# Performance work log

Hardware: AMD Instinct MI355X
Metric: run time of the kernel (lower is better)

## Reference

```python
import jax, jax.numpy as jnp
import numpy as np


def setup_inputs() -> dict:
    key = jax.random.key(0)
    k1, k2, k3, k4 = jax.random.split(key, 4)
    N, F, E, M = 50000, 128, 1600000, 1024
    return {
        "molec_feature_vectures": jax.random.normal(k1, (N, F), dtype=jnp.float32),
        "W": jax.random.normal(k2, (F, F), dtype=jnp.float32),
        "mo_neighbour_indices": jax.random.randint(k3, (2, E), 0, N, dtype=jnp.int64),
        "mo_mol_id": jax.random.randint(k4, (E,), 0, M, dtype=jnp.int64),
        "n_output": M,
    }


def reference(molec_feature_vectures, W, mo_neighbour_indices, mo_mol_id, n_output):
    # Gather endpoint features for each neighbor pair: [E, F]
    fi = molec_feature_vectures[mo_neighbour_indices[0]]
    fj = molec_feature_vectures[mo_neighbour_indices[1]]
    # Symmetric bilinear form (mode='pes'): s_n = fi_n . (W + W^T) . fj_n
    Ws = W + W.T  # [F, F]
    # Fuse as (fi @ Ws) * fj summed over F to avoid a 3-operand einsum blowup
    scalars = jnp.einsum('ni,ij,nj->n', fi, Ws, fj)  # [E]
    # Segment-sum per molecule
    res = jax.ops.segment_sum(scalars, mo_mol_id, num_segments=n_output)  # [M]
    return res
```

## Files before the change

kernel.cpp:

```cpp
#include <hip/hip_runtime.h>
#include <hip/hip_bf16.h>

#define FDIM 128
#define BROWS 32
#define NBLK 128
#define NSLICE 32

typedef __attribute__((ext_vector_type(8))) short short8v;
typedef __attribute__((ext_vector_type(4))) float f32x4;
typedef __attribute__((ext_vector_type(2))) _Float16 half2v;

static __device__ __forceinline__ unsigned short f2bf(float x) {
    unsigned u = __float_as_uint(x);
    unsigned r = 0x7fffu + ((u >> 16) & 1u);
    return (unsigned short)((u + r) >> 16);
}
static __device__ __forceinline__ float bf2f(unsigned short h) {
    return __uint_as_float((unsigned)h << 16);
}
static __device__ __forceinline__ void split2(float v, short& h, short& l) {
    unsigned short hh = f2bf(v);
    h = (short)hh;
    l = (short)f2bf(v - bf2f(hh));
}

static __device__ __forceinline__ half2v u2h(unsigned u) {
    union { unsigned u; half2v h; } c; c.u = u; return c.h;
}
static __device__ __forceinline__ unsigned pack2h(float a, float b) {
    union { unsigned u; half2v h; } c;
    c.h[0] = (_Float16)a; c.h[1] = (_Float16)b; return c.u;
}
static __device__ __forceinline__ unsigned short f2h(float x) {
    union { unsigned short s; _Float16 h; } c; c.h = (_Float16)x; return c.s;
}
static __device__ __forceinline__ float fdot2(half2v a, half2v b, float c) {
#if defined(__has_builtin) && __has_builtin(__builtin_amdgcn_fdot2)
    return __builtin_amdgcn_fdot2(a, b, c, false);
#else
    return fmaf((float)a[1], (float)b[1], fmaf((float)a[0], (float)b[0], c));
#endif
}

__global__ void make_ws2(const float* __restrict__ W,
                         unsigned short* __restrict__ WsH,
                         unsigned short* __restrict__ WsL) {
    int idx = blockIdx.x * 256 + threadIdx.x;
    int i = idx >> 7, j = idx & 127;
    float w = W[idx] + W[j * 128 + i];
    short h, l;
    split2(w, h, l);
    WsH[idx] = (unsigned short)h;
    WsL[idx] = (unsigned short)l;
}

__global__ __launch_bounds__(512, 4) void gemm_mfma(
    const float* __restrict__ Fm,
    const unsigned short* __restrict__ WsH, const unsigned short* __restrict__ WsL,
    unsigned short* __restrict__ Gh, int N) {
    __shared__ __align__(16) unsigned short sH[128 * 136];
    __shared__ __align__(16) unsigned short sL[128 * 136];

    for (int k = threadIdx.x; k < 128 * 16; k += 512) {
        int i = k >> 4, g = k & 15;
        *(uint4*)((char*)sH + i * 272 + g * 16) =
            *(const uint4*)((const char*)WsH + i * 256 + g * 16);
        *(uint4*)((char*)sL + i * 272 + g * 16) =
            *(const uint4*)((const char*)WsL + i * 256 + g * 16);
    }
    __syncthreads();

    const int wid  = threadIdx.x >> 6;
    const int lane = threadIdx.x & 63;
    const int ar   = lane & 15;
    const int kg   = lane >> 4;
    const int row0 = blockIdx.x * 128 + wid * 16;
    const int gr   = row0 + ar;
    const bool rv  = gr < N;
    const float* fp = Fm + (size_t)gr * FDIM;

    f32x4 acc[8];
#pragma unroll
    for (int t = 0; t < 8; ++t) acc[t] = (f32x4){0.f, 0.f, 0.f, 0.f};

#pragma unroll
    for (int ks = 0; ks < 4; ++ks) {
        const int k0 = ks * 32 + kg * 8;
        float4 fa = make_float4(0.f, 0.f, 0.f, 0.f);
        float4 fb = make_float4(0.f, 0.f, 0.f, 0.f);
        if (rv) {
            fa = *(const float4*)(fp + k0);
            fb = *(const float4*)(fp + k0 + 4);
        }
        short8v ah, al;
        {
            short h, l;
            split2(fa.x, h, l); ah[0] = h; al[0] = l;
            split2(fa.y, h, l); ah[1] = h; al[1] = l;
            split2(fa.z, h, l); ah[2] = h; al[2] = l;
            split2(fa.w, h, l); ah[3] = h; al[3] = l;
            split2(fb.x, h, l); ah[4] = h; al[4] = l;
            split2(fb.y, h, l); ah[5] = h; al[5] = l;
            split2(fb.z, h, l); ah[6] = h; al[6] = l;
            split2(fb.w, h, l); ah[7] = h; al[7] = l;
        }
#pragma unroll
        for (int ct = 0; ct < 8; ++ct) {
            const short8v bh = *(const short8v*)(sH + (ct * 16 + ar) * 136 + k0);
            const short8v bl = *(const short8v*)(sL + (ct * 16 + ar) * 136 + k0);
            acc[ct] = __builtin_amdgcn_mfma_f32_16x16x32_bf16(ah, bh, acc[ct], 0, 0, 0);
            acc[ct] = __builtin_amdgcn_mfma_f32_16x16x32_bf16(ah, bl, acc[ct], 0, 0, 0);
            acc[ct] = __builtin_amdgcn_mfma_f32_16x16x32_bf16(al, bh, acc[ct], 0, 0, 0);
        }
    }

#pragma unroll
    for (int r = 0; r < 4; ++r) {
        const int orow = row0 + kg * 4 + r;
        if (orow < N) {
#pragma unroll
            for (int ct = 0; ct < 8; ++ct)
                Gh[(size_t)orow * FDIM + ct * 16 + ar] = f2h(acc[ct][r]);
        }
    }
}

__global__ __launch_bounds__(1024) void k_hist(const int* __restrict__ idx, int E,
                                               int nb, unsigned* __restrict__ M) {
    extern __shared__ unsigned cnt[];
    for (int i = threadIdx.x; i < nb; i += 1024) cnt[i] = 0;
    __syncthreads();
    int chunk = (E + NBLK - 1) / NBLK;
    int s = blockIdx.x * chunk;
    int e_end = min(E, s + chunk);
    for (int e = s + threadIdx.x; e < e_end; e += 1024) {
        int i1 = idx[E + e];
        atomicAdd(&cnt[i1 >> 5], 1u);
    }
    __syncthreads();
    for (int i = threadIdx.x; i < nb; i += 1024)
        M[(size_t)blockIdx.x * nb + i] = cnt[i];
}

__global__ __launch_bounds__(256) void k_mscan2(unsigned* __restrict__ M, int nb,
                                                unsigned* __restrict__ tot) {
    int b = blockIdx.x * 4 + (threadIdx.x >> 6);
    int lane = threadIdx.x & 63;
    if (b >= nb) return;
    unsigned m0 = M[(size_t)(2 * lane + 0) * nb + b];
    unsigned m1 = M[(size_t)(2 * lane + 1) * nb + b];
    unsigned s = m0 + m1;
    unsigned incl = s;
#pragma unroll
    for (int d = 1; d < 64; d <<= 1) {
        unsigned u = __shfl_up(incl, d, 64);
        if (lane >= d) incl += u;
    }
    unsigned run = incl - s;
    M[(size_t)(2 * lane + 0) * nb + b] = run; run += m0;
    M[(size_t)(2 * lane + 1) * nb + b] = run;
    if (lane == 63) tot[b] = incl;
}

__global__ __launch_bounds__(256) void k_bscan(const unsigned* __restrict__ tot, int nb,
                                               unsigned* __restrict__ bucketStart) {
    __shared__ unsigned wS[4];
    int t = threadIdx.x;
    unsigned v0, v1, v2, v3, v4, v5, v6, v7;
    int b0 = t * 8;
    v0 = (b0 + 0 < nb) ? tot[b0 + 0] : 0u;
    v1 = (b0 + 1 < nb) ? tot[b0 + 1] : 0u;
    v2 = (b0 + 2 < nb) ? tot[b0 + 2] : 0u;
    v3 = (b0 + 3 < nb) ? tot[b0 + 3] : 0u;
    v4 = (b0 + 4 < nb) ? tot[b0 + 4] : 0u;
    v5 = (b0 + 5 < nb) ? tot[b0 + 5] : 0u;
    v6 = (b0 + 6 < nb) ? tot[b0 + 6] : 0u;
    v7 = (b0 + 7 < nb) ? tot[b0 + 7] : 0u;
    unsigned l0 = 0, l1 = v0, l2 = l1 + v1, l3 = l2 + v2, l4 = l3 + v3,
             l5 = l4 + v4, l6 = l5 + v5, l7 = l6 + v6;
    unsigned s = l7 + v7;
    int lane = t & 63, wid = t >> 6;
    unsigned incl = s;
    for (int d = 1; d < 64; d <<= 1) {
        unsigned u = __shfl_up(incl, d, 64);
        if (lane >= d) incl += u;
    }
    if (lane == 63) wS[wid] = incl;
    __syncthreads();
    unsigned wOff = 0;
    for (int i = 0; i < wid; ++i) wOff += wS[i];
    unsigned base = wOff + incl - s;
    if (b0 + 0 < nb) bucketStart[b0 + 0] = base + l0;
    if (b0 + 1 < nb) bucketStart[b0 + 1] = base + l1;
    if (b0 + 2 < nb) bucketStart[b0 + 2] = base + l2;
    if (b0 + 3 < nb) bucketStart[b0 + 3] = base + l3;
    if (b0 + 4 < nb) bucketStart[b0 + 4] = base + l4;
    if (b0 + 5 < nb) bucketStart[b0 + 5] = base + l5;
    if (b0 + 6 < nb) bucketStart[b0 + 6] = base + l6;
    if (b0 + 7 < nb) bucketStart[b0 + 7] = base + l7;
    if (t == 255) bucketStart[nb] = base + s;
}

__global__ __launch_bounds__(1024) void k_scatter(const int* __restrict__ idx,
                                                  const int* __restrict__ mol, int E,
                                                  int nb, const unsigned* __restrict__ M,
                                                  const unsigned* __restrict__ bucketStart,
                                                  unsigned* __restrict__ sortedE) {
    extern __shared__ unsigned cur[];
    for (int i = threadIdx.x; i < nb; i += 1024)
        cur[i] = M[(size_t)blockIdx.x * nb + i] + bucketStart[i];
    __syncthreads();
    int chunk = (E + NBLK - 1) / NBLK;
    int s = blockIdx.x * chunk;
    int e_end = min(E, s + chunk);
    for (int e = s + threadIdx.x; e < e_end; e += 1024) {
        int i0 = idx[e];
        int i1 = idx[E + e];
        int m  = mol[e];
        int b  = i1 >> 5;
        int loc = i1 & 31;
        unsigned pos = atomicAdd(&cur[b], 1u);
        sortedE[pos] = (unsigned)i0 | ((unsigned)m << 16) | ((unsigned)loc << 26);
    }
}

__global__ __launch_bounds__(512, 6) void edge_kernel(
    const unsigned short* __restrict__ Gh, const float* __restrict__ Fm,
    const unsigned* __restrict__ sortedE, const unsigned* __restrict__ bucketStart,
    float* __restrict__ part, int N, int Mout) {
    __shared__ __align__(16) unsigned short sFrow[BROWS * FDIM];
    __shared__ float smol[1024];

    const int b = blockIdx.x;
    const int row0 = b * BROWS;
    const int nrow = min(BROWS, N - row0);

    for (int k = threadIdx.x; k < nrow * 16; k += 512) {
        int r = k >> 4, g = k & 15;
        const float4* src = (const float4*)(Fm + (size_t)(row0 + r) * FDIM + g * 8);
        float4 v0 = src[0], v1 = src[1];
        uint4 u;
        u.x = pack2h(v0.x, v0.y);
        u.y = pack2h(v0.z, v0.w);
        u.z = pack2h(v1.x, v1.y);
        u.w = pack2h(v1.z, v1.w);
        *(uint4*)(sFrow + r * FDIM + g * 8) = u;
    }
    for (int i = threadIdx.x; i < 1024; i += 512) smol[i] = 0.f;
    __syncthreads();

    const int s = (int)bucketStart[b];
    const int e_end = (int)bucketStart[b + 1];
    const int lane = threadIdx.x & 63;
    const int sub  = lane >> 4;
    const int t16  = lane & 15;
    const int off16 = t16 * 8;
    const int wid  = threadIdx.x >> 6;

#define DOT8(p, g, f) \
    p = fdot2(u2h((g).x), u2h((f).x), p); \
    p = fdot2(u2h((g).y), u2h((f).y), p); \
    p = fdot2(u2h((g).z), u2h((f).z), p); \
    p = fdot2(u2h((g).w), u2h((f).w), p);

    int base = s + wid * 16;
    unsigned pk0 = 0u, pk1 = 0u, pk2 = 0u, pk3 = 0u;
    if (base + sub < e_end)      pk0 = sortedE[base + sub];
    if (base + 4 + sub < e_end)  pk1 = sortedE[base + 4 + sub];
    if (base + 8 + sub < e_end)  pk2 = sortedE[base + 8 + sub];
    if (base + 12 + sub < e_end) pk3 = sortedE[base + 12 + sub];

    while (base < e_end) {
        const int nbase = base + 128;
        unsigned npk0 = 0u, npk1 = 0u, npk2 = 0u, npk3 = 0u;
        if (nbase + sub < e_end)      npk0 = sortedE[nbase + sub];
        if (nbase + 4 + sub < e_end)  npk1 = sortedE[nbase + 4 + sub];
        if (nbase + 8 + sub < e_end)  npk2 = sortedE[nbase + 8 + sub];
        if (nbase + 12 + sub < e_end) npk3 = sortedE[nbase + 12 + sub];

        const uint4 g0 = *(const uint4*)(Gh + (size_t)(pk0 & 0xffffu) * FDIM + off16);
        const uint4 g1 = *(const uint4*)(Gh + (size_t)(pk1 & 0xffffu) * FDIM + off16);
        const uint4 g2 = *(const uint4*)(Gh + (size_t)(pk2 & 0xffffu) * FDIM + off16);
        const uint4 g3 = *(const uint4*)(Gh + (size_t)(pk3 & 0xffffu) * FDIM + off16);
        const uint4 f0 = *(const uint4*)(sFrow + (pk0 >> 26) * FDIM + off16);
        const uint4 f1 = *(const uint4*)(sFrow + (pk1 >> 26) * FDIM + off16);
        const uint4 f2 = *(const uint4*)(sFrow + (pk2 >> 26) * FDIM + off16);
        const uint4 f3 = *(const uint4*)(sFrow + (pk3 >> 26) * FDIM + off16);

        float p0 = 0.f, p1 = 0.f, p2 = 0.f, p3 = 0.f;
        DOT8(p0, g0, f0);
        DOT8(p1, g1, f1);
        DOT8(p2, g2, f2);
        DOT8(p3, g3, f3);

        p0 += __shfl_xor(p0, 1, 16);
        p1 += __shfl_xor(p1, 1, 16);
        p2 += __shfl_xor(p2, 1, 16);
        p3 += __shfl_xor(p3, 1, 16);
        p0 += __shfl_xor(p0, 2, 16);
        p1 += __shfl_xor(p1, 2, 16);
        p2 += __shfl_xor(p2, 2, 16);
        p3 += __shfl_xor(p3, 2, 16);
        p0 += __shfl_xor(p0, 4, 16);
        p1 += __shfl_xor(p1, 4, 16);
        p2 += __shfl_xor(p2, 4, 16);
        p3 += __shfl_xor(p3, 4, 16);
        p0 += __shfl_xor(p0, 8, 16);
        p1 += __shfl_xor(p1, 8, 16);
        p2 += __shfl_xor(p2, 8, 16);
        p3 += __shfl_xor(p3, 8, 16);

        if (t16 == 0) {
            if (base + sub < e_end)      atomicAdd(&smol[(pk0 >> 16) & 0x3ff], p0);
            if (base + 4 + sub < e_end)  atomicAdd(&smol[(pk1 >> 16) & 0x3ff], p1);
            if (base + 8 + sub < e_end)  atomicAdd(&smol[(pk2 >> 16) & 0x3ff], p2);
            if (base + 12 + sub < e_end) atomicAdd(&smol[(pk3 >> 16) & 0x3ff], p3);
        }
        pk0 = npk0; pk1 = npk1; pk2 = npk2; pk3 = npk3;
        base = nbase;
    }
#undef DOT8
    __syncthreads();

    float* prow = part + (size_t)b * 1024;
    for (int i = threadIdx.x; i < Mout; i += 512) prow[i] = smol[i];
}

__global__ __launch_bounds__(256) void k_red1(const float* __restrict__ part, int nb,
                                              float* __restrict__ partial, int Mout) {
    int gid = blockIdx.x * 256 + threadIdx.x;
    int m = gid & 1023;
    int sl = gid >> 10;
    int per = (nb + NSLICE - 1) / NSLICE;
    int b0 = sl * per;
    int b1 = min(nb, b0 + per);
    float s = 0.f;
    if (m < Mout) {
        for (int b = b0; b < b1; ++b) s += part[(size_t)b * 1024 + m];
    }
    partial[sl * 1024 + m] = s;
}

__global__ __launch_bounds__(256) void k_red2(const float* __restrict__ partial,
                                              float* __restrict__ out, int Mout) {
    int m = blockIdx.x * 256 + threadIdx.x;
    if (m < Mout) {
        float s = 0.f;
        for (int sl = 0; sl < NSLICE; ++sl) s += partial[sl * 1024 + m];
        out[m] = s;
    }
}

extern "C" void kernel_launch(void* const* d_in, const int* in_sizes, int n_in,
                              void* d_out, int out_size, void* d_ws, size_t ws_size,
                              hipStream_t stream) {
    const float* Fm = (const float*)d_in[0];
    const float* W  = (const float*)d_in[1];
    const int* idx  = (const int*)d_in[2];
    const int* mol  = (const int*)d_in[3];
    float* out = (float*)d_out;

    const int N = in_sizes[0] / FDIM;
    const int E = in_sizes[3];

    const int nb = (N + BROWS - 1) / BROWS;

    char* ws = (char*)d_ws;
    size_t o = 0;
    unsigned short* WsH = (unsigned short*)(ws + o); o += 32 * 1024;
    unsigned short* WsL = (unsigned short*)(ws + o); o += 32 * 1024;
    unsigned short* Gh = (unsigned short*)(ws + o);  o += ((size_t)N * FDIM * 2 + 255) & ~(size_t)255;
    unsigned* sortedE = (unsigned*)(ws + o);         o += ((size_t)E * 4 + 255) & ~(size_t)255;
    unsigned* M = (unsigned*)(ws + o);               o += ((size_t)NBLK * nb * 4 + 255) & ~(size_t)255;
    unsigned* tot = (unsigned*)(ws + o);             o += ((size_t)nb * 4 + 255) & ~(size_t)255;
    unsigned* bucketStart = (unsigned*)(ws + o);     o += ((size_t)(nb + 1) * 4 + 255) & ~(size_t)255;
    float* part = (float*)(ws + o);                  o += (size_t)nb * 1024 * sizeof(float);
    float* partial = (float*)(ws + o);               o += NSLICE * 1024 * sizeof(float);

    make_ws2<<<64, 256, 0, stream>>>(W, WsH, WsL);
    gemm_mfma<<<(N + 127) / 128, 512, 0, stream>>>(Fm, WsH, WsL, Gh, N);

    size_t smem = (size_t)nb * 4;
    k_hist<<<NBLK, 1024, smem, stream>>>(idx, E, nb, M);
    k_mscan2<<<(nb + 3) / 4, 256, 0, stream>>>(M, nb, tot);
    k_bscan<<<1, 256, 0, stream>>>(tot, nb, bucketStart);
    k_scatter<<<NBLK, 1024, smem, stream>>>(idx, mol, E, nb, M, bucketStart, sortedE);

    edge_kernel<<<nb, 512, 0, stream>>>(Gh, Fm, sortedE, bucketStart, part, N, out_size);

    k_red1<<<NSLICE * 4, 256, 0, stream>>>(part, nb, partial, out_size);
    k_red2<<<(out_size + 255) / 256, 256, 0, stream>>>(partial, out, out_size);
}
```

Baseline: 199.1 us.

## Fuse Ws build into histogram kernel, halve sort blocks, deepen edge-loop prefetch

Merges the W+W^T bf16 split kernel into the histogram kernel as 16 extra blocks, removing one launch. NBLK drops from 128 to 64, so the histogram scan reads one count per lane instead of two, and the scatter uses fewer but longer blocks. The edge kernel now prefetches Gh rows one iteration ahead and edge records two iterations ahead, which hides gather latency at the cost of more registers. Fewer histogram and scatter blocks may reduce parallelism in those phases.

Result: slower. 207.0 us (+4.0%).

```diff
diff --git a/kernel.cpp b/kernel.cpp
--- a/kernel.cpp
+++ b/kernel.cpp
@@ -3,7 +3,7 @@
 
 #define FDIM 128
 #define BROWS 32
-#define NBLK 128
+#define NBLK 64
 #define NSLICE 32
 
 typedef __attribute__((ext_vector_type(8))) short short8v;
@@ -42,16 +42,33 @@
 #endif
 }
 
-__global__ void make_ws2(const float* __restrict__ W,
-                         unsigned short* __restrict__ WsH,
-                         unsigned short* __restrict__ WsL) {
-    int idx = blockIdx.x * 256 + threadIdx.x;
-    int i = idx >> 7, j = idx & 127;
-    float w = W[idx] + W[j * 128 + i];
-    short h, l;
-    split2(w, h, l);
-    WsH[idx] = (unsigned short)h;
-    WsL[idx] = (unsigned short)l;
+__global__ __launch_bounds__(1024) void k_ws_hist(
+    const float* __restrict__ W,
+    unsigned short* __restrict__ WsH, unsigned short* __restrict__ WsL,
+    const int* __restrict__ idx, int E, int nb, unsigned* __restrict__ M) {
+    if (blockIdx.x >= NBLK) {
+        int i2 = (blockIdx.x - NBLK) * 1024 + threadIdx.x;
+        int i = i2 >> 7, j = i2 & 127;
+        float w = W[i2] + W[j * 128 + i];
+        short h, l;
+        split2(w, h, l);
+        WsH[i2] = (unsigned short)h;
+        WsL[i2] = (unsigned short)l;
+        return;
+    }
+    extern __shared__ unsigned cnt[];
+    for (int i = threadIdx.x; i < nb; i += 1024) cnt[i] = 0;
+    __syncthreads();
+    int chunk = (E + NBLK - 1) / NBLK;
+    int s = blockIdx.x * chunk;
+    int e_end = min(E, s + chunk);
+    for (int e = s + threadIdx.x; e < e_end; e += 1024) {
+        int i1 = idx[E + e];
+        atomicAdd(&cnt[i1 >> 5], 1u);
+    }
+    __syncthreads();
+    for (int i = threadIdx.x; i < nb; i += 1024)
+        M[(size_t)blockIdx.x * nb + i] = cnt[i];
 }
 
 __global__ __launch_bounds__(512, 4) void gemm_mfma(
@@ -125,40 +142,19 @@
     }
 }
 
-__global__ __launch_bounds__(1024) void k_hist(const int* __restrict__ idx, int E,
-                                               int nb, unsigned* __restrict__ M) {
-    extern __shared__ unsigned cnt[];
-    for (int i = threadIdx.x; i < nb; i += 1024) cnt[i] = 0;
-    __syncthreads();
-    int chunk = (E + NBLK - 1) / NBLK;
-    int s = blockIdx.x * chunk;
-    int e_end = min(E, s + chunk);
-    for (int e = s + threadIdx.x; e < e_end; e += 1024) {
-        int i1 = idx[E + e];
-        atomicAdd(&cnt[i1 >> 5], 1u);
-    }
-    __syncthreads();
-    for (int i = threadIdx.x; i < nb; i += 1024)
-        M[(size_t)blockIdx.x * nb + i] = cnt[i];
-}
-
 __global__ __launch_bounds__(256) void k_mscan2(unsigned* __restrict__ M, int nb,
                                                 unsigned* __restrict__ tot) {
     int b = blockIdx.x * 4 + (threadIdx.x >> 6);
     int lane = threadIdx.x & 63;
     if (b >= nb) return;
-    unsigned m0 = M[(size_t)(2 * lane + 0) * nb + b];
-    unsigned m1 = M[(size_t)(2 * lane + 1) * nb + b];
-    unsigned s = m0 + m1;
-    unsigned incl = s;
+    unsigned m0 = M[(size_t)lane * nb + b];
+    unsigned incl = m0;
 #pragma unroll
     for (int d = 1; d < 64; d <<= 1) {
         unsigned u = __shfl_up(incl, d, 64);
         if (lane >= d) incl += u;
     }
-    unsigned run = incl - s;
-    M[(size_t)(2 * lane + 0) * nb + b] = run; run += m0;
-    M[(size_t)(2 * lane + 1) * nb + b] = run;
+    M[(size_t)lane * nb + b] = incl - m0;
     if (lane == 63) tot[b] = incl;
 }
 
@@ -264,34 +260,47 @@
     p = fdot2(u2h((g).w), u2h((f).w), p);
 
     int base = s + wid * 16;
-    unsigned pk0 = 0u, pk1 = 0u, pk2 = 0u, pk3 = 0u;
-    if (base + sub < e_end)      pk0 = sortedE[base + sub];
-    if (base + 4 + sub < e_end)  pk1 = sortedE[base + 4 + sub];
-    if (base + 8 + sub < e_end)  pk2 = sortedE[base + 8 + sub];
-    if (base + 12 + sub < e_end) pk3 = sortedE[base + 12 + sub];
+
+    unsigned pc0 = 0u, pc1 = 0u, pc2 = 0u, pc3 = 0u;
+    unsigned pn0 = 0u, pn1 = 0u, pn2 = 0u, pn3 = 0u;
+    if (base + sub < e_end)      pc0 = sortedE[base + sub];
+    if (base + 4 + sub < e_end)  pc1 = sortedE[base + 4 + sub];
+    if (base + 8 + sub < e_end)  pc2 = sortedE[base + 8 + sub];
+    if (base + 12 + sub < e_end) pc3 = sortedE[base + 12 + sub];
+    {
+        const int nx = base + 128;
+        if (nx + sub < e_end)      pn0 = sortedE[nx + sub];
+        if (nx + 4 + sub < e_end)  pn1 = sortedE[nx + 4 + sub];
+        if (nx + 8 + sub < e_end)  pn2 = sortedE[nx + 8 + sub];
+        if (nx + 12 + sub < e_end) pn3 = sortedE[nx + 12 + sub];
+    }
+    uint4 gc0 = *(const uint4*)(Gh + (size_t)(pc0 & 0xffffu) * FDIM + off16);
+    uint4 gc1 = *(const uint4*)(Gh + (size_t)(pc1 & 0xffffu) * FDIM + off16);
+    uint4 gc2 = *(const uint4*)(Gh + (size_t)(pc2 & 0xffffu) * FDIM + off16);
+    uint4 gc3 = *(const uint4*)(Gh + (size_t)(pc3 & 0xffffu) * FDIM + off16);
 
     while (base < e_end) {
-        const int nbase = base + 128;
-        unsigned npk0 = 0u, npk1 = 0u, npk2 = 0u, npk3 = 0u;
-        if (nbase + sub < e_end)      npk0 = sortedE[nbase + sub];
-        if (nbase + 4 + sub < e_end)  npk1 = sortedE[nbase + 4 + sub];
-        if (nbase + 8 + sub < e_end)  npk2 = sortedE[nbase + 8 + sub];
-        if (nbase + 12 + sub < e_end) npk3 = sortedE[nbase + 12 + sub];
-
-        const uint4 g0 = *(const uint4*)(Gh + (size_t)(pk0 & 0xffffu) * FDIM + off16);
-        const uint4 g1 = *(const uint4*)(Gh + (size_t)(pk1 & 0xffffu) * FDIM + off16);
-        const uint4 g2 = *(const uint4*)(Gh + (size_t)(pk2 & 0xffffu) * FDIM + off16);
-        const uint4 g3 = *(const uint4*)(Gh + (size_t)(pk3 & 0xffffu) * FDIM + off16);
-        const uint4 f0 = *(const uint4*)(sFrow + (pk0 >> 26) * FDIM + off16);
-        const uint4 f1 = *(const uint4*)(sFrow + (pk1 >> 26) * FDIM + off16);
-        const uint4 f2 = *(const uint4*)(sFrow + (pk2 >> 26) * FDIM + off16);
-        const uint4 f3 = *(const uint4*)(sFrow + (pk3 >> 26) * FDIM + off16);
+        const uint4 gn0 = *(const uint4*)(Gh + (size_t)(pn0 & 0xffffu) * FDIM + off16);
+        const uint4 gn1 = *(const uint4*)(Gh + (size_t)(pn1 & 0xffffu) * FDIM + off16);
+        const uint4 gn2 = *(const uint4*)(Gh + (size_t)(pn2 & 0xffffu) * FDIM + off16);
+        const uint4 gn3 = *(const uint4*)(Gh + (size_t)(pn3 & 0xffffu) * FDIM + off16);
+        const int pf = base + 256;
+        unsigned p20 = 0u, p21 = 0u, p22 = 0u, p23 = 0u;
+        if (pf + sub < e_end)      p20 = sortedE[pf + sub];
+        if (pf + 4 + sub < e_end)  p21 = sortedE[pf + 4 + sub];
+        if (pf + 8 + sub < e_end)  p22 = sortedE[pf + 8 + sub];
+        if (pf + 12 + sub < e_end) p23 = sortedE[pf + 12 + sub];
+
+        const uint4 f0 = *(const uint4*)(sFrow + (pc0 >> 26) * FDIM + off16);
+        const uint4 f1 = *(const uint4*)(sFrow + (pc1 >> 26) * FDIM + off16);
+        const uint4 fv2 = *(const uint4*)(sFrow + (pc2 >> 26) * FDIM + off16);
+        const uint4 f3 = *(const uint4*)(sFrow + (pc3 >> 26) * FDIM + off16);
 
         float p0 = 0.f, p1 = 0.f, p2 = 0.f, p3 = 0.f;
-        DOT8(p0, g0, f0);
-        DOT8(p1, g1, f1);
-        DOT8(p2, g2, f2);
-        DOT8(p3, g3, f3);
+        DOT8(p0, gc0, f0);
+        DOT8(p1, gc1, f1);
+        DOT8(p2, gc2, fv2);
+        DOT8(p3, gc3, f3);
 
         p0 += __shfl_xor(p0, 1, 16);
         p1 += __shfl_xor(p1, 1, 16);
@@ -311,13 +320,15 @@
         p3 += __shfl_xor(p3, 8, 16);
 
         if (t16 == 0) {
-            if (base + sub < e_end)      atomicAdd(&smol[(pk0 >> 16) & 0x3ff], p0);
-            if (base + 4 + sub < e_end)  atomicAdd(&smol[(pk1 >> 16) & 0x3ff], p1);
-            if (base + 8 + sub < e_end)  atomicAdd(&smol[(pk2 >> 16) & 0x3ff], p2);
-            if (base + 12 + sub < e_end) atomicAdd(&smol[(pk3 >> 16) & 0x3ff], p3);
+            if (base + sub < e_end)      atomicAdd(&smol[(pc0 >> 16) & 0x3ff], p0);
+            if (base + 4 + sub < e_end)  atomicAdd(&smol[(pc1 >> 16) & 0x3ff], p1);
+            if (base + 8 + sub < e_end)  atomicAdd(&smol[(pc2 >> 16) & 0x3ff], p2);
+            if (base + 12 + sub < e_end) atomicAdd(&smol[(pc3 >> 16) & 0x3ff], p3);
         }
-        pk0 = npk0; pk1 = npk1; pk2 = npk2; pk3 = npk3;
-        base = nbase;
+        gc0 = gn0; gc1 = gn1; gc2 = gn2; gc3 = gn3;
+        pc0 = pn0; pc1 = pn1; pc2 = pn2; pc3 = pn3;
+        pn0 = p20; pn1 = p21; pn2 = p22; pn3 = p23;
+        base += 128;
     }
 #undef DOT8
     __syncthreads();
@@ -377,11 +388,9 @@
     float* part = (float*)(ws + o);                  o += (size_t)nb * 1024 * sizeof(float);
     float* partial = (float*)(ws + o);               o += NSLICE * 1024 * sizeof(float);
 
-    make_ws2<<<64, 256, 0, stream>>>(W, WsH, WsL);
+    size_t smem = (size_t)nb * 4;
+    k_ws_hist<<<NBLK + 16, 1024, smem, stream>>>(W, WsH, WsL, idx, E, nb, M);
     gemm_mfma<<<(N + 127) / 128, 512, 0, stream>>>(Fm, WsH, WsL, Gh, N);
-
-    size_t smem = (size_t)nb * 4;
-    k_hist<<<NBLK, 1024, smem, stream>>>(idx, E, nb, M);
     k_mscan2<<<(nb + 3) / 4, 256, 0, stream>>>(M, nb, tot);
     k_bscan<<<1, 256, 0, stream>>>(tot, nb, bucketStart);
     k_scatter<<<NBLK, 1024, smem, stream>>>(idx, mol, E, nb, M, bucketStart, sortedE);
```
